# Kernel tuning notes

Hardware: AMD Instinct MI355X
Metric: run time of the kernel (lower is better)

The kernel has to match this reference:

```python
import jax, jax.numpy as jnp
import numpy as np
import math

ROPE_THETA = 10000.0


def apply_rope(x, positions):
    # x: [B, H, S, d_k], positions: [S]
    d_k = x.shape[-1]
    inv_freq = 1.0 / (ROPE_THETA ** (jnp.arange(0, d_k, 2, dtype=jnp.float32) / d_k))  # [d_k/2]
    angles = positions.astype(jnp.float32)[:, None] * inv_freq[None, :]  # [S, d_k/2]
    cos = jnp.cos(angles)
    sin = jnp.sin(angles)
    x1 = x[..., 0::2]
    x2 = x[..., 1::2]
    r1 = x1 * cos - x2 * sin
    r2 = x1 * sin + x2 * cos
    out = jnp.stack([r1, r2], axis=-1)  # interleave pairs back
    return out.reshape(x.shape)


def setup_inputs() -> dict:
    key = jax.random.key(0)
    k1, k2, k3 = jax.random.split(key, 3)
    B, S, D = 4, 2048, 1024
    x = jax.random.normal(k1, (B, S, D), dtype=jnp.float32)
    token_positions = jnp.arange(S, dtype=jnp.int32)
    w_qkv = jax.random.normal(k2, (3 * D, D), dtype=jnp.float32) * (1.0 / math.sqrt(D))
    w_o = jax.random.normal(k3, (D, D), dtype=jnp.float32) * (1.0 / math.sqrt(D))
    return {"x": x, "token_positions": token_positions, "w_qkv": w_qkv, "w_o": w_o}


def reference(x, token_positions, w_qkv, w_o):
    B, S, D = x.shape
    H = 16
    d_k = D // H
    qkv = jnp.einsum('bsd,ed->bse', x, w_qkv)  # [B, S, 3D]
    # rearrange '... s (stack h dk) -> stack ... h s dk'
    qkv = qkv.reshape(B, S, 3, H, d_k)
    q = jnp.transpose(qkv[:, :, 0], (0, 2, 1, 3))  # [B, H, S, dk]
    k = jnp.transpose(qkv[:, :, 1], (0, 2, 1, 3))
    v = jnp.transpose(qkv[:, :, 2], (0, 2, 1, 3))
    q = apply_rope(q, token_positions)
    k = apply_rope(k, token_positions)
    scores = jnp.einsum('bhqd,bhkd->bhqk', q, k) / math.sqrt(d_k)
    causal = jnp.tril(jnp.ones((S, S), dtype=bool))
    scores = jnp.where(causal[None, None], scores, -jnp.inf)
    attn = jax.nn.softmax(scores, axis=-1)
    out = jnp.einsum('bhqk,bhkd->bhqd', attn, v)  # [B, H, S, dk]
    out = jnp.transpose(out, (0, 2, 1, 3)).reshape(B, S, D)
    return jnp.einsum('bsd,ed->bse', out, w_o)
```

## Files before the change

kernel.cpp:

```cpp
#include <hip/hip_runtime.h>
#include <hip/hip_bf16.h>
#include <math.h>

typedef __bf16 bf16_t;
typedef __attribute__((ext_vector_type(8))) __bf16 bf16x8;
typedef __attribute__((ext_vector_type(4))) __bf16 bf16x4;
typedef __attribute__((ext_vector_type(4))) float f32x4;

#define MFMA_16x16x32(A_, B_, C_) __builtin_amdgcn_mfma_f32_16x16x32_bf16((A_), (B_), (C_), 0, 0, 0)

#define Bsz 4
#define Ssz 2048
#define Dsz 1024
#define Hh 16
#define DKd 64
#define Mrows (Bsz * Ssz)
#define N1 (3 * Dsz)
#define KD Dsz

__global__ void cvt_f32_bf16_kernel(const float* __restrict__ src, bf16_t* __restrict__ dst, int n4) {
  int i = blockIdx.x * blockDim.x + threadIdx.x;
  if (i >= n4) return;
  float4 v = reinterpret_cast<const float4*>(src)[i];
  bf16x4 o = {(bf16_t)v.x, (bf16_t)v.y, (bf16_t)v.z, (bf16_t)v.w};
  reinterpret_cast<bf16x4*>(dst)[i] = o;
}

__global__ void rope_tab_kernel(const int* __restrict__ pos, float2* __restrict__ tab) {
  int i = blockIdx.x * blockDim.x + threadIdx.x;
  if (i >= Ssz * 32) return;
  int s = i >> 5, f = i & 31;
  float inv_freq = powf(10000.0f, -(float)(2 * f) / 64.0f);
  float a = (float)pos[s] * inv_freq;
  tab[i] = make_float2(cosf(a), sinf(a));
}

template <int EPI>
__global__ __launch_bounds__(256, 2) void gemm_tn_kernel(
    const bf16_t* __restrict__ A, const bf16_t* __restrict__ Bt, int Kdim, int ldcN,
    bf16_t* __restrict__ qb, bf16_t* __restrict__ kb, bf16_t* __restrict__ vtb,
    const float2* __restrict__ tab, float* __restrict__ fout) {
  constexpr int LDA = 40;
  __shared__ __align__(16) bf16_t As[128 * LDA];
  __shared__ __align__(16) bf16_t Bs[128 * LDA];
  const int t = threadIdx.x;
  const int w = t >> 6, l = t & 63;
  const int lr = l & 15, lk = l >> 4;
  const int wm = w >> 1, wn = w & 1;
  const int m0 = blockIdx.y * 128, n0 = blockIdx.x * 128;

  const int srow = t >> 2;
  const int scol = (t & 3) * 8;
  const bf16_t* gA0 = A + (size_t)(m0 + srow) * Kdim + scol;
  const bf16_t* gA1 = A + (size_t)(m0 + 64 + srow) * Kdim + scol;
  const bf16_t* gB0 = Bt + (size_t)(n0 + srow) * Kdim + scol;
  const bf16_t* gB1 = Bt + (size_t)(n0 + 64 + srow) * Kdim + scol;
  bf16_t* sA0 = As + srow * LDA + scol;
  bf16_t* sA1 = As + (64 + srow) * LDA + scol;
  bf16_t* sB0 = Bs + srow * LDA + scol;
  bf16_t* sB1 = Bs + (64 + srow) * LDA + scol;

  f32x4 acc[4][4] = {};

  for (int kt = 0; kt < Kdim; kt += 32) {
    bf16x8 ra0 = *reinterpret_cast<const bf16x8*>(gA0 + kt);
    bf16x8 ra1 = *reinterpret_cast<const bf16x8*>(gA1 + kt);
    bf16x8 rb0 = *reinterpret_cast<const bf16x8*>(gB0 + kt);
    bf16x8 rb1 = *reinterpret_cast<const bf16x8*>(gB1 + kt);
    __syncthreads();
    *reinterpret_cast<bf16x8*>(sA0) = ra0;
    *reinterpret_cast<bf16x8*>(sA1) = ra1;
    *reinterpret_cast<bf16x8*>(sB0) = rb0;
    *reinterpret_cast<bf16x8*>(sB1) = rb1;
    __syncthreads();
    bf16x8 af[4], bfv[4];
#pragma unroll
    for (int m = 0; m < 4; ++m)
      af[m] = *reinterpret_cast<const bf16x8*>(As + (wm * 64 + m * 16 + lr) * LDA + lk * 8);
#pragma unroll
    for (int n = 0; n < 4; ++n)
      bfv[n] = *reinterpret_cast<const bf16x8*>(Bs + (wn * 64 + n * 16 + lr) * LDA + lk * 8);
#pragma unroll
    for (int m = 0; m < 4; ++m)
#pragma unroll
      for (int n = 0; n < 4; ++n)
        acc[m][n] = MFMA_16x16x32(af[m], bfv[n], acc[m][n]);
  }

  if (EPI == 0) {
#pragma unroll
    for (int n = 0; n < 4; ++n) {
      const int col = n0 + wn * 64 + n * 16 + lr;
      const int sect = col >> 10;
      const int h = (col >> 6) & 15;
      const int dk = col & 63;
#pragma unroll
      for (int m = 0; m < 4; ++m) {
        const int growb = m0 + wm * 64 + m * 16 + lk * 4;
#pragma unroll
        for (int r = 0; r < 4; ++r) {
          const int grow = growb + r;
          const int bb = grow >> 11;
          const int s = grow & (Ssz - 1);
          float v = acc[m][n][r];
          if (sect < 2) {
            const float pv = __shfl_xor(v, 1);
            const float2 cs = tab[(s << 5) | (dk >> 1)];
            float vr = (dk & 1) ? (pv * cs.y + v * cs.x) : (v * cs.x - pv * cs.y);
            const size_t idx = ((size_t)((bb * Hh + h) * Ssz + s)) * DKd + dk;
            if (sect == 0)
              qb[idx] = (bf16_t)(vr * 0.125f);
            else
              kb[idx] = (bf16_t)vr;
          } else {
            vtb[((size_t)(bb * Hh + h) * DKd + dk) * Ssz + s] = (bf16_t)v;
          }
        }
      }
    }
  } else {
#pragma unroll
    for (int m = 0; m < 4; ++m)
#pragma unroll
      for (int r = 0; r < 4; ++r) {
        const int grow = m0 + wm * 64 + m * 16 + lk * 4 + r;
        float* op = fout + (size_t)grow * ldcN + n0 + wn * 64 + lr;
#pragma unroll
        for (int n = 0; n < 4; ++n) op[n * 16] = acc[m][n][r];
      }
  }
}

__global__ __launch_bounds__(256, 3) void attn_kernel(
    const bf16_t* __restrict__ qb, const bf16_t* __restrict__ kb,
    const bf16_t* __restrict__ vtb, bf16_t* __restrict__ aout) {
  __shared__ __align__(16) bf16_t Ks[64 * 64];
  __shared__ __align__(16) bf16_t Vs[64 * 64];
  const int t = threadIdx.x, w = t >> 6, l = t & 63;
  const int lr = l & 15, lk = l >> 4;
  const int bid = blockIdx.x;
  const int bh = (bid & 7) * 8 + ((bid >> 3) & 7);
  const int qt = 15 - (bid >> 6);
  const int q0 = qt * 128;
  const int sub0 = q0 + w * 32;

  const bf16_t* qbase = qb + ((size_t)bh * Ssz + sub0) * DKd;
  bf16x8 qf[2][2];
#pragma unroll
  for (int s = 0; s < 2; ++s) {
    qf[s][0] = *reinterpret_cast<const bf16x8*>(qbase + (s * 16 + lr) * DKd + lk * 8);
    qf[s][1] = *reinterpret_cast<const bf16x8*>(qbase + (s * 16 + lr) * DKd + 32 + lk * 8);
  }

  f32x4 o[2][4] = {};
  float mrow[2] = {-INFINITY, -INFINITY};
  float lsum[2] = {0.f, 0.f};

  const int srow = t >> 2;
  const int scc = (t & 3) * 2;
  const bf16_t* kg = kb + ((size_t)bh * Ssz + srow) * DKd + scc * 8;
  const bf16_t* vg = vtb + ((size_t)bh * DKd + srow) * Ssz + scc * 8;
  bf16_t* ksw0 = Ks + srow * 64 + ((scc ^ (srow & 7)) * 8);
  bf16_t* ksw1 = Ks + srow * 64 + (((scc + 1) ^ (srow & 7)) * 8);
  bf16_t* vw[4];
#pragma unroll
  for (int u = 0; u < 2; ++u) {
    const int c = scc + u;
    const int B = 32 * (c >> 2) + 16 * (c & 1) + 4 * ((c & 3) >> 1);
    const int ch = B >> 3, off = B & 7;
    vw[2 * u] = Vs + srow * 64 + ((ch ^ (srow & 7)) * 8) + off;
    vw[2 * u + 1] = Vs + srow * 64 + (((ch + 1) ^ (srow & 7)) * 8) + off;
  }

  const int kvend = q0 + 128;
  bf16x8 pk0 = *reinterpret_cast<const bf16x8*>(kg);
  bf16x8 pk1 = *reinterpret_cast<const bf16x8*>(kg + 8);
  bf16x8 pv0 = *reinterpret_cast<const bf16x8*>(vg);
  bf16x8 pv1 = *reinterpret_cast<const bf16x8*>(vg + 8);

  for (int kv = 0; kv < kvend; kv += 64) {
    __syncthreads();
    *reinterpret_cast<bf16x8*>(ksw0) = pk0;
    *reinterpret_cast<bf16x8*>(ksw1) = pk1;
    *reinterpret_cast<bf16x4*>(vw[0]) = __builtin_shufflevector(pv0, pv0, 0, 1, 2, 3);
    *reinterpret_cast<bf16x4*>(vw[1]) = __builtin_shufflevector(pv0, pv0, 4, 5, 6, 7);
    *reinterpret_cast<bf16x4*>(vw[2]) = __builtin_shufflevector(pv1, pv1, 0, 1, 2, 3);
    *reinterpret_cast<bf16x4*>(vw[3]) = __builtin_shufflevector(pv1, pv1, 4, 5, 6, 7);
    __syncthreads();
    if (kv + 64 < kvend) {
      pk0 = *reinterpret_cast<const bf16x8*>(kg + (size_t)(kv + 64) * DKd);
      pk1 = *reinterpret_cast<const bf16x8*>(kg + (size_t)(kv + 64) * DKd + 8);
      pv0 = *reinterpret_cast<const bf16x8*>(vg + kv + 64);
      pv1 = *reinterpret_cast<const bf16x8*>(vg + kv + 64 + 8);
    }
#pragma unroll
    for (int s = 0; s < 2; ++s) {
      const int subrow = sub0 + s * 16;
      if (kv > subrow + 15) continue;
      f32x4 sa[4];
#pragma unroll
      for (int n = 0; n < 4; ++n) {
        const int R = n * 16 + lr;
        const bf16x8 a0 = *reinterpret_cast<const bf16x8*>(Ks + R * 64 + ((lk ^ (R & 7)) * 8));
        const bf16x8 a1 = *reinterpret_cast<const bf16x8*>(Ks + R * 64 + (((lk + 4) ^ (R & 7)) * 8));
        f32x4 z = {};
        z = MFMA_16x16x32(a0, qf[s][0], z);
        z = MFMA_16x16x32(a1, qf[s][1], z);
        sa[n] = z;
      }
      if (kv + 63 > subrow) {
        const int qrow = subrow + lr;
        const int kbase = kv + lk * 4;
#pragma unroll
        for (int n = 0; n < 4; ++n)
#pragma unroll
          for (int r = 0; r < 4; ++r)
            if (kbase + n * 16 + r > qrow) sa[n][r] = -INFINITY;
      }
      float mx = fmaxf(fmaxf(fmaxf(sa[0][0], sa[0][1]), fmaxf(sa[0][2], sa[0][3])),
                       fmaxf(fmaxf(sa[1][0], sa[1][1]), fmaxf(sa[1][2], sa[1][3])));
      mx = fmaxf(mx, fmaxf(fmaxf(fmaxf(sa[2][0], sa[2][1]), fmaxf(sa[2][2], sa[2][3])),
                           fmaxf(fmaxf(sa[3][0], sa[3][1]), fmaxf(sa[3][2], sa[3][3]))));
      mx = fmaxf(mx, __shfl_xor(mx, 16));
      mx = fmaxf(mx, __shfl_xor(mx, 32));
      const float mnew = fmaxf(mrow[s], mx);
      const float scl = __expf(mrow[s] - mnew);
      mrow[s] = mnew;
      float ps = 0.f;
#pragma unroll
      for (int n = 0; n < 4; ++n)
#pragma unroll
        for (int r = 0; r < 4; ++r) {
          const float p = __expf(sa[n][r] - mnew);
          sa[n][r] = p;
          ps += p;
        }
      lsum[s] = lsum[s] * scl + ps;
#pragma unroll
      for (int n = 0; n < 4; ++n)
#pragma unroll
        for (int r = 0; r < 4; ++r) o[s][n][r] *= scl;
      bf16x8 pb0, pb1;
#pragma unroll
      for (int r = 0; r < 4; ++r) {
        pb0[r] = (bf16_t)sa[0][r];
        pb0[4 + r] = (bf16_t)sa[1][r];
        pb1[r] = (bf16_t)sa[2][r];
        pb1[4 + r] = (bf16_t)sa[3][r];
      }
#pragma unroll
      for (int n = 0; n < 4; ++n) {
        const int R = n * 16 + lr;
        const bf16x8 v0 = *reinterpret_cast<const bf16x8*>(Vs + R * 64 + ((lk ^ (R & 7)) * 8));
        const bf16x8 v1 = *reinterpret_cast<const bf16x8*>(Vs + R * 64 + (((lk + 4) ^ (R & 7)) * 8));
        o[s][n] = MFMA_16x16x32(v0, pb0, o[s][n]);
        o[s][n] = MFMA_16x16x32(v1, pb1, o[s][n]);
      }
    }
  }
  const int b_ = bh >> 4, h_ = bh & 15;
#pragma unroll
  for (int s = 0; s < 2; ++s) {
    float sm = lsum[s];
    sm += __shfl_xor(sm, 16);
    sm += __shfl_xor(sm, 32);
    const float inv = 1.0f / sm;
    const int qrow = sub0 + s * 16 + lr;
    bf16_t* op = aout + ((size_t)b_ * Ssz + qrow) * Dsz + h_ * DKd + lk * 4;
#pragma unroll
    for (int n = 0; n < 4; ++n) {
      const bf16x4 ov = {(bf16_t)(o[s][n][0] * inv), (bf16_t)(o[s][n][1] * inv),
                         (bf16_t)(o[s][n][2] * inv), (bf16_t)(o[s][n][3] * inv)};
      *reinterpret_cast<bf16x4*>(op + n * 16) = ov;
    }
  }
}

extern "C" void kernel_launch(void* const* d_in, const int* in_sizes, int n_in,
                              void* d_out, int out_size, void* d_ws, size_t ws_size,
                              hipStream_t stream) {
  const float* x = (const float*)d_in[0];
  const int* pos = (const int*)d_in[1];
  const float* wqkv = (const float*)d_in[2];
  const float* wo = (const float*)d_in[3];
  float* out = (float*)d_out;

  bf16_t* xb = (bf16_t*)d_ws;
  bf16_t* wqkvb = xb + (size_t)Mrows * KD;
  bf16_t* wob = wqkvb + (size_t)N1 * KD;
  bf16_t* qbuf = wob + (size_t)Dsz * KD;
  bf16_t* kbuf = qbuf + (size_t)64 * Ssz * DKd;
  bf16_t* vtb = kbuf + (size_t)64 * Ssz * DKd;
  float2* tab = (float2*)(vtb + (size_t)64 * Ssz * DKd);
  bf16_t* aout = xb;

  {
    int n4 = Mrows * KD / 4;
    cvt_f32_bf16_kernel<<<(n4 + 255) / 256, 256, 0, stream>>>(x, xb, n4);
  }
  {
    int n4 = N1 * KD / 4;
    cvt_f32_bf16_kernel<<<(n4 + 255) / 256, 256, 0, stream>>>(wqkv, wqkvb, n4);
  }
  {
    int n4 = Dsz * KD / 4;
    cvt_f32_bf16_kernel<<<(n4 + 255) / 256, 256, 0, stream>>>(wo, wob, n4);
  }
  rope_tab_kernel<<<(Ssz * 32 + 255) / 256, 256, 0, stream>>>(pos, tab);

  gemm_tn_kernel<0><<<dim3(N1 / 128, Mrows / 128), 256, 0, stream>>>(
      xb, wqkvb, KD, 0, qbuf, kbuf, vtb, tab, nullptr);

  attn_kernel<<<dim3(16 * 64), 256, 0, stream>>>(qbuf, kbuf, vtb, aout);

  gemm_tn_kernel<1><<<dim3(Dsz / 128, Mrows / 128), 256, 0, stream>>>(
      aout, wob, KD, Dsz, nullptr, nullptr, nullptr, nullptr, out);
}
```

Baseline: 220.2 us.

## Load GEMM tiles directly into LDS with XOR swizzle and raise occupancy

The GEMM main loop now uses global_load_lds to copy A and B tiles straight from global memory into LDS, skipping the staging through registers. The padded LDS layout is replaced by an unpadded one with an XOR swizzle on 16-byte chunks to avoid bank conflicts, and a trailing barrier protects the buffer before it is reused. Launch bounds move to three blocks per CU, which limits registers per thread and risks spills. There is still no double buffering, so load latency stays exposed behind the barriers.

```diff
diff --git a/kernel.cpp b/kernel.cpp
--- a/kernel.cpp
+++ b/kernel.cpp
@@ -36,13 +36,12 @@
 }
 
 template <int EPI>
-__global__ __launch_bounds__(256, 2) void gemm_tn_kernel(
+__global__ __launch_bounds__(256, 3) void gemm_tn_kernel(
     const bf16_t* __restrict__ A, const bf16_t* __restrict__ Bt, int Kdim, int ldcN,
     bf16_t* __restrict__ qb, bf16_t* __restrict__ kb, bf16_t* __restrict__ vtb,
     const float2* __restrict__ tab, float* __restrict__ fout) {
-  constexpr int LDA = 40;
-  __shared__ __align__(16) bf16_t As[128 * LDA];
-  __shared__ __align__(16) bf16_t Bs[128 * LDA];
+  __shared__ __align__(16) bf16_t As[128 * 32];
+  __shared__ __align__(16) bf16_t Bs[128 * 32];
   const int t = threadIdx.x;
   const int w = t >> 6, l = t & 63;
   const int lr = l & 15, lk = l >> 4;
@@ -50,41 +49,36 @@
   const int m0 = blockIdx.y * 128, n0 = blockIdx.x * 128;
 
   const int srow = t >> 2;
-  const int scol = (t & 3) * 8;
-  const bf16_t* gA0 = A + (size_t)(m0 + srow) * Kdim + scol;
-  const bf16_t* gA1 = A + (size_t)(m0 + 64 + srow) * Kdim + scol;
-  const bf16_t* gB0 = Bt + (size_t)(n0 + srow) * Kdim + scol;
-  const bf16_t* gB1 = Bt + (size_t)(n0 + 64 + srow) * Kdim + scol;
-  bf16_t* sA0 = As + srow * LDA + scol;
-  bf16_t* sA1 = As + (64 + srow) * LDA + scol;
-  bf16_t* sB0 = Bs + srow * LDA + scol;
-  bf16_t* sB1 = Bs + (64 + srow) * LDA + scol;
+  const int schunk = (t & 3) ^ ((t >> 3) & 3);
+  const bf16_t* gA = A + (size_t)(m0 + srow) * Kdim + schunk * 8;
+  const bf16_t* gB = Bt + (size_t)(n0 + srow) * Kdim + schunk * 8;
+  bf16_t* sA0 = As + (size_t)(w * 16) * 32;
+  bf16_t* sA1 = As + (size_t)(64 + w * 16) * 32;
+  bf16_t* sB0 = Bs + (size_t)(w * 16) * 32;
+  bf16_t* sB1 = Bs + (size_t)(64 + w * 16) * 32;
 
   f32x4 acc[4][4] = {};
 
   for (int kt = 0; kt < Kdim; kt += 32) {
-    bf16x8 ra0 = *reinterpret_cast<const bf16x8*>(gA0 + kt);
-    bf16x8 ra1 = *reinterpret_cast<const bf16x8*>(gA1 + kt);
-    bf16x8 rb0 = *reinterpret_cast<const bf16x8*>(gB0 + kt);
-    bf16x8 rb1 = *reinterpret_cast<const bf16x8*>(gB1 + kt);
-    __syncthreads();
-    *reinterpret_cast<bf16x8*>(sA0) = ra0;
-    *reinterpret_cast<bf16x8*>(sA1) = ra1;
-    *reinterpret_cast<bf16x8*>(sB0) = rb0;
-    *reinterpret_cast<bf16x8*>(sB1) = rb1;
+    __builtin_amdgcn_global_load_lds(gA + kt, sA0, 16, 0, 0);
+    __builtin_amdgcn_global_load_lds(gA + (size_t)64 * Kdim + kt, sA1, 16, 0, 0);
+    __builtin_amdgcn_global_load_lds(gB + kt, sB0, 16, 0, 0);
+    __builtin_amdgcn_global_load_lds(gB + (size_t)64 * Kdim + kt, sB1, 16, 0, 0);
     __syncthreads();
     bf16x8 af[4], bfv[4];
+    const int rsw = (lr >> 1) & 3;
 #pragma unroll
     for (int m = 0; m < 4; ++m)
-      af[m] = *reinterpret_cast<const bf16x8*>(As + (wm * 64 + m * 16 + lr) * LDA + lk * 8);
+      af[m] = *reinterpret_cast<const bf16x8*>(As + (wm * 64 + m * 16 + lr) * 32 + ((lk ^ rsw) * 8));
 #pragma unroll
     for (int n = 0; n < 4; ++n)
-      bfv[n] = *reinterpret_cast<const bf16x8*>(Bs + (wn * 64 + n * 16 + lr) * LDA + lk * 8);
+      bfv[n] = *reinterpret_cast<const bf16x8*>(Bs + (wn * 64 + n * 16 + lr) * 32 + ((lk ^ rsw) * 8));
 #pragma unroll
     for (int m = 0; m < 4; ++m)
 #pragma unroll
       for (int n = 0; n < 4; ++n)
         acc[m][n] = MFMA_16x16x32(af[m], bfv[n], acc[m][n]);
+    __syncthreads();
   }
 
   if (EPI == 0) {
```

Measured after the change: 213.5 us. 3.1% less time.
